# Performance work log

Measured on AMD Instinct MI355X. Metric: run time of the kernel, lower is better.

The kernel has to match this reference:

```python
import jax, jax.numpy as jnp
import numpy as np

N_GRAPHS = 128
NEG_SLOPE = 0.2
BN_EPS = 1e-5


def _gatv2(x, edge_index, edge_attr, Wl, bl, Wr, br, We, att, bias):
    # PyG GATv2Conv, heads=1, add_self_loops=True with fill_value='mean' for edge_attr.
    N = x.shape[0]
    src, dst = edge_index[0], edge_index[1]
    ones = jnp.ones(src.shape[0], dtype=x.dtype)
    deg = jax.ops.segment_sum(ones, dst, num_segments=N)
    loop_attr = jax.ops.segment_sum(edge_attr, dst, num_segments=N) / jnp.maximum(deg, 1.0)[:, None]
    idx = jnp.arange(N)
    src = jnp.concatenate([src, idx])
    dst = jnp.concatenate([dst, idx])
    ea = jnp.concatenate([edge_attr, loop_attr], axis=0)
    xl = x @ Wl + bl            # source projection [N, out]
    xr = x @ Wr + br            # target projection [N, out]
    h = jax.nn.leaky_relu(xl[src] + xr[dst] + ea @ We, NEG_SLOPE)  # [E, out]
    e = h @ att                 # attention logits [E]
    m = jax.ops.segment_max(e, dst, num_segments=N)
    ex = jnp.exp(e - m[dst])
    den = jax.ops.segment_sum(ex, dst, num_segments=N)
    alpha = ex / den[dst]       # per-destination softmax
    out = jax.ops.segment_sum(xl[src] * alpha[:, None], dst, num_segments=N)
    return out + bias


def setup_inputs() -> dict:
    key = jax.random.key(0)
    ks = jax.random.split(key, 32)
    N, E, FIN, ED = 16384, 131072, 256, 32

    def lin(k, fi, fo):
        return jax.random.normal(k, (fi, fo), jnp.float32) / np.sqrt(fi)

    d = {}
    d['x'] = jax.random.normal(ks[0], (N, FIN), jnp.float32)
    d['edge_index'] = jax.random.randint(ks[1], (2, E), 0, N)
    d['edge_attr'] = jax.random.normal(ks[2], (E, ED), jnp.float32)
    d['batch'] = jnp.sort(jax.random.randint(ks[3], (N,), 0, N_GRAPHS))
    dims = [(FIN, 512), (512, 1024), (1024, 256)]
    ki = 4
    for i, (fi, fo) in enumerate(dims, 1):
        d[f'Wl{i}'] = lin(ks[ki], fi, fo); ki += 1
        d[f'bl{i}'] = jnp.zeros((fo,), jnp.float32)
        d[f'Wr{i}'] = lin(ks[ki], fi, fo); ki += 1
        d[f'br{i}'] = jnp.zeros((fo,), jnp.float32)
        d[f'We{i}'] = lin(ks[ki], ED, fo); ki += 1
        d[f'att{i}'] = jax.random.normal(ks[ki], (fo,), jnp.float32) / np.sqrt(fo); ki += 1
        d[f'bc{i}'] = jnp.zeros((fo,), jnp.float32)
    d['fc1_w'] = lin(ks[ki], 256, 64); ki += 1
    d['fc1_b'] = jnp.zeros((64,), jnp.float32)
    d['bn_g'] = jnp.ones((64,), jnp.float32)
    d['bn_b'] = jnp.zeros((64,), jnp.float32)
    d['fc2_w'] = lin(ks[ki], 64, 1); ki += 1
    d['fc2_b'] = jnp.zeros((1,), jnp.float32)
    return d


def reference(x, edge_index, edge_attr, batch,
              Wl1, bl1, Wr1, br1, We1, att1, bc1,
              Wl2, bl2, Wr2, br2, We2, att2, bc2,
              Wl3, bl3, Wr3, br3, We3, att3, bc3,
              fc1_w, fc1_b, bn_g, bn_b, fc2_w, fc2_b):
    h = jax.nn.relu(_gatv2(x, edge_index, edge_attr, Wl1, bl1, Wr1, br1, We1, att1, bc1))
    h = jax.nn.relu(_gatv2(h, edge_index, edge_attr, Wl2, bl2, Wr2, br2, We2, att2, bc2))
    h = jax.nn.relu(_gatv2(h, edge_index, edge_attr, Wl3, bl3, Wr3, br3, We3, att3, bc3))
    # global mean pool over graphs
    cnt = jax.ops.segment_sum(jnp.ones(h.shape[0], h.dtype), batch, num_segments=N_GRAPHS)
    pooled = jax.ops.segment_sum(h, batch, num_segments=N_GRAPHS) / jnp.maximum(cnt, 1.0)[:, None]
    # dropout in eval mode (identity)
    z = pooled @ fc1_w + fc1_b
    mu = jnp.mean(z, axis=0)
    var = jnp.var(z, axis=0)
    z = (z - mu) / jnp.sqrt(var + BN_EPS) * bn_g + bn_b
    z = jax.nn.relu(z)
    return z @ fc2_w + fc2_b
```

## Files before the change

kernel.cpp:

```cpp
#include <hip/hip_runtime.h>
#include <hip/hip_bf16.h>
#include <math.h>

#define NEG_SLOPE 0.2f

typedef short bf16x8 __attribute__((ext_vector_type(8)));
typedef float f32x4 __attribute__((ext_vector_type(4)));

__device__ __forceinline__ float lrelu(float x){ return x >= 0.f ? x : NEG_SLOPE * x; }
__device__ __forceinline__ unsigned short f2bf(float f){
  __hip_bfloat16 h = __float2bfloat16(f);
  return *(unsigned short*)&h;
}
__device__ __forceinline__ float bf2f(unsigned short u){
  return __uint_as_float((unsigned)u << 16);
}
__device__ __forceinline__ void up8(uint4 q, float* f){
  f[0] = __uint_as_float(q.x << 16); f[1] = __uint_as_float(q.x & 0xffff0000u);
  f[2] = __uint_as_float(q.y << 16); f[3] = __uint_as_float(q.y & 0xffff0000u);
  f[4] = __uint_as_float(q.z << 16); f[5] = __uint_as_float(q.z & 0xffff0000u);
  f[6] = __uint_as_float(q.w << 16); f[7] = __uint_as_float(q.w & 0xffff0000u);
}

__device__ __forceinline__ void gload_lds16(const unsigned short* g, unsigned short* l){
  __builtin_amdgcn_global_load_lds(
      (const __attribute__((address_space(1))) unsigned int*)g,
      (__attribute__((address_space(3))) unsigned int*)l, 16, 0, 0);
}

__global__ void k_deg(const int* __restrict__ ei, int* __restrict__ deg, int E){
  int e = blockIdx.x * 256 + threadIdx.x;
  if (e >= E) return;
  atomicAdd(&deg[ei[E + e]], 1);
}

__global__ void k_scan(const int* __restrict__ deg, int* __restrict__ row_start, int N){
  __shared__ int s[256];
  int t = threadIdx.x;
  int base = t * 64;
  int sum = 0;
  for (int i = 0; i < 64; ++i) sum += deg[base + i] + 1;
  s[t] = sum;
  __syncthreads();
  for (int off = 1; off < 256; off <<= 1){
    int v = (t >= off) ? s[t - off] : 0;
    __syncthreads();
    s[t] += v;
    __syncthreads();
  }
  int run = s[t] - sum;
  for (int i = 0; i < 64; ++i){ row_start[base + i] = run; run += deg[base + i] + 1; }
  if (t == 255) row_start[N] = run;
}

__global__ void k_csr_build(const int* __restrict__ ei, const int* __restrict__ row_start,
                            int* __restrict__ fill, int* __restrict__ csr_src,
                            int* __restrict__ csr_eid, int* __restrict__ csr_dst,
                            int N, int E){
  int idx = blockIdx.x * 256 + threadIdx.x;
  if (idx < N){
    int p = row_start[idx];
    csr_src[p] = idx;
    csr_eid[p] = E;
    csr_dst[p] = idx;
  } else {
    int e = idx - N;
    if (e >= E) return;
    int dst = ei[E + e];
    int p = row_start[dst] + 1 + atomicAdd(&fill[dst], 1);
    csr_src[p] = ei[e];
    csr_eid[p] = e;
    csr_dst[p] = dst;
  }
}

__global__ void k_eaprep(const float* __restrict__ ea, const int* __restrict__ csr_eid,
                         const int* __restrict__ row_start,
                         unsigned short* __restrict__ ea_perm, int N, int Eaug, int E){
  int idx = blockIdx.x * 256 + threadIdx.x;
  if (idx < N * 32){
    int n = idx >> 5, k = idx & 31;
    int rs = row_start[n], re = row_start[n + 1];
    float sum = 0.f;
    for (int i = rs + 1; i < re; ++i)
      sum += ea[(size_t)csr_eid[i] * 32 + k];
    float d = (float)max(re - rs - 1, 1);
    ea_perm[(size_t)rs * 32 + k] = f2bf(sum / d);
  } else {
    int j = idx - N * 32;
    int p = j >> 3, q = j & 7;
    if (p >= Eaug) return;
    int e = csr_eid[p];
    if (e >= E) return;
    float4 v = ((const float4*)(ea + (size_t)e * 32))[q];
    ushort4 o;
    o.x = f2bf(v.x); o.y = f2bf(v.y); o.z = f2bf(v.z); o.w = f2bf(v.w);
    *(ushort4*)&ea_perm[(size_t)p * 32 + q * 4] = o;
  }
}

__global__ void k_cvt_bf16(const float* __restrict__ in, unsigned short* __restrict__ out, int n4){
  int idx = blockIdx.x * 256 + threadIdx.x;
  if (idx >= n4) return;
  float4 v = *(const float4*)&in[idx * 4];
  ushort4 o;
  o.x = f2bf(v.x); o.y = f2bf(v.y); o.z = f2bf(v.z); o.w = f2bf(v.w);
  *(ushort4*)&out[idx * 4] = o;
}

__global__ __launch_bounds__(256) void k_transpose2_bf16(const float* __restrict__ W0,
    const float* __restrict__ W1, unsigned short* __restrict__ Wt0,
    unsigned short* __restrict__ Wt1, int K, int N){
  __shared__ float tile[64][65];
  const float* W = blockIdx.z ? W1 : W0;
  unsigned short* Wt = blockIdx.z ? Wt1 : Wt0;
  int n0 = blockIdx.x * 64, k0 = blockIdx.y * 64;
  int col = threadIdx.x & 63, rq = threadIdx.x >> 6;
  #pragma unroll
  for (int i = 0; i < 16; ++i){
    int r = rq * 16 + i;
    tile[r][col] = W[(size_t)(k0 + r) * N + n0 + col];
  }
  __syncthreads();
  #pragma unroll
  for (int i = 0; i < 16; ++i){
    int r = rq * 16 + i;
    Wt[(size_t)(n0 + r) * K + k0 + col] = f2bf(tile[col][r]);
  }
}

__global__ void k_transpose_we(const float* __restrict__ We, unsigned short* __restrict__ WeT, int FO){
  int idx = blockIdx.x * 256 + threadIdx.x;
  if (idx >= 32 * FO) return;
  int k = idx / FO, n = idx % FO;
  WeT[n * 32 + k] = f2bf(We[idx]);
}

__global__ void k_mfma_gemm2(const unsigned short* __restrict__ A,
    const unsigned short* __restrict__ BtL, const unsigned short* __restrict__ BtR,
    const float* __restrict__ biasL, const float* __restrict__ biasR,
    unsigned short* __restrict__ CL, unsigned short* __restrict__ CR, int FO, int K){
  __shared__ unsigned short lds[16384];
  unsigned short* As0 = lds;
  unsigned short* As1 = lds + 4096;
  unsigned short* Bs0 = lds + 8192;
  unsigned short* Bs1 = lds + 12288;
  const unsigned short* Bt = blockIdx.z ? BtR : BtL;
  const float* bias = blockIdx.z ? biasR : biasL;
  unsigned short* C = blockIdx.z ? CR : CL;
  int t = threadIdx.x;
  int mb = blockIdx.x, nb = blockIdx.y;
  int lane = t & 63, w = t >> 6;
  int wm = (w & 1) * 64, wn = (w >> 1) * 64;
  int lo = lane & 15, hi = lane >> 4;
  int srow = w * 32 + (lane >> 2);
  int scol = (lane & 3) * 8;
  const unsigned short* Ap0 = A + (size_t)(mb * 128 + srow) * K + scol;
  const unsigned short* Ap1 = Ap0 + (size_t)16 * K;
  const unsigned short* Bp0 = Bt + (size_t)(nb * 128 + srow) * K + scol;
  const unsigned short* Bp1 = Bp0 + (size_t)16 * K;
  unsigned short* Ad00 = As0 + (w * 32) * 32;
  unsigned short* Ad01 = As0 + (w * 32 + 16) * 32;
  unsigned short* Ad10 = As1 + (w * 32) * 32;
  unsigned short* Ad11 = As1 + (w * 32 + 16) * 32;
  unsigned short* Bd00 = Bs0 + (w * 32) * 32;
  unsigned short* Bd01 = Bs0 + (w * 32 + 16) * 32;
  unsigned short* Bd10 = Bs1 + (w * 32) * 32;
  unsigned short* Bd11 = Bs1 + (w * 32 + 16) * 32;
  f32x4 acc[4][4] = {};
  for (int k0 = 0; k0 < K; k0 += 64){
    gload_lds16(Ap0 + k0, Ad00);
    gload_lds16(Ap1 + k0, Ad01);
    gload_lds16(Ap0 + k0 + 32, Ad10);
    gload_lds16(Ap1 + k0 + 32, Ad11);
    gload_lds16(Bp0 + k0, Bd00);
    gload_lds16(Bp1 + k0, Bd01);
    gload_lds16(Bp0 + k0 + 32, Bd10);
    gload_lds16(Bp1 + k0 + 32, Bd11);
    __syncthreads();
    #pragma unroll
    for (int ks = 0; ks < 2; ++ks){
      const unsigned short* Asx = ks ? As1 : As0;
      const unsigned short* Bsx = ks ? Bs1 : Bs0;
      bf16x8 af[4], bfr[4];
      #pragma unroll
      for (int i = 0; i < 4; ++i){
        af[i]  = *(const bf16x8*)&Asx[(wm + i * 16 + lo) * 32 + hi * 8];
        bfr[i] = *(const bf16x8*)&Bsx[(wn + i * 16 + lo) * 32 + hi * 8];
      }
      #pragma unroll
      for (int mi = 0; mi < 4; ++mi)
        #pragma unroll
        for (int ni = 0; ni < 4; ++ni)
          acc[mi][ni] = __builtin_amdgcn_mfma_f32_16x16x32_bf16(af[mi], bfr[ni], acc[mi][ni], 0, 0, 0);
    }
    __syncthreads();
  }
  #pragma unroll
  for (int ni = 0; ni < 4; ++ni){
    int col = wn + ni * 16 + lo;
    float bv = bias[nb * 128 + col];
    #pragma unroll
    for (int mi = 0; mi < 4; ++mi){
      int row = wm + mi * 16 + hi * 4;
      #pragma unroll
      for (int r = 0; r < 4; ++r)
        lds[(row + r) * 128 + col] = f2bf(acc[mi][ni][r] + bv);
    }
  }
  __syncthreads();
  #pragma unroll
  for (int q = 0; q < 8; ++q){
    int idx = q * 256 + t;
    int row = idx >> 4;
    int cs = (idx & 15) * 8;
    *(float4*)&C[(size_t)(mb * 128 + row) * FO + nb * 128 + cs] = *(float4*)&lds[row * 128 + cs];
  }
}

template<int TILES>
__global__ __launch_bounds__(256, 3) void k_logit(const unsigned short* __restrict__ Ap,
    const unsigned short* __restrict__ WeT, const unsigned short* __restrict__ XL,
    const unsigned short* __restrict__ XRb, const int* __restrict__ csr_src,
    const int* __restrict__ csr_dst, const float* __restrict__ att,
    float* __restrict__ logit){
  const int FO = TILES * 128;
  const int EWS = 140;
  __shared__ unsigned short ewt[128 * EWS];
  __shared__ int s_soff[128], s_doff[128];
  int t = threadIdx.x;
  int base = blockIdx.x * 128;
  if (t < 128){
    s_soff[t] = csr_src[base + t] * FO;
    s_doff[t] = csr_dst[base + t] * FO;
  }
  int lane = t & 63, w = t >> 6;
  int wm = (w & 1) * 64, wn = (w >> 1) * 64;
  int lo = lane & 15, hi = lane >> 4;
  bf16x8 af[4];
  #pragma unroll
  for (int i = 0; i < 4; ++i)
    af[i] = *(const bf16x8*)&Ap[(size_t)(base + wm + i * 16 + lo) * 32 + hi * 8];
  int grp = t >> 4, li = t & 15;
  __syncthreads();
  int soff8[8], doff8[8];
  #pragma unroll
  for (int e8 = 0; e8 < 8; ++e8){
    soff8[e8] = s_soff[grp * 8 + e8] + li * 8;
    doff8[e8] = s_doff[grp * 8 + e8] + li * 8;
  }
  float part[8] = {};
  #pragma unroll 1
  for (int nb = 0; nb < TILES; ++nb){
    bf16x8 bfr[4];
    #pragma unroll
    for (int i = 0; i < 4; ++i)
      bfr[i] = *(const bf16x8*)&WeT[(size_t)(nb * 128 + wn + i * 16 + lo) * 32 + hi * 8];
    __syncthreads();
    #pragma unroll
    for (int ni = 0; ni < 4; ++ni){
      f32x4 acc[4] = {};
      #pragma unroll
      for (int mi = 0; mi < 4; ++mi)
        acc[mi] = __builtin_amdgcn_mfma_f32_16x16x32_bf16(af[mi], bfr[ni], acc[mi], 0, 0, 0);
      int col = wn + ni * 16 + lo;
      #pragma unroll
      for (int mi = 0; mi < 4; ++mi){
        int row = wm + mi * 16 + hi * 4;
        #pragma unroll
        for (int r = 0; r < 4; ++r)
          ewt[(row + r) * EWS + col] = f2bf(acc[mi][r]);
      }
    }
    __syncthreads();
    float4 aA = *(const float4*)&att[nb * 128 + li * 8];
    float4 aB = *(const float4*)&att[nb * 128 + li * 8 + 4];
    #pragma unroll
    for (int e8 = 0; e8 < 8; ++e8){
      int r = grp * 8 + e8;
      uint4 qx = *(const uint4*)&XL [(size_t)soff8[e8] + nb * 128];
      uint4 qr = *(const uint4*)&XRb[(size_t)doff8[e8] + nb * 128];
      uint4 qe = *(const uint4*)&ewt[r * EWS + li * 8];
      float fx[8], fr8[8], fe[8];
      up8(qx, fx); up8(qr, fr8); up8(qe, fe);
      float s;
      s  = aA.x * lrelu(fx[0] + fr8[0] + fe[0]);
      s += aA.y * lrelu(fx[1] + fr8[1] + fe[1]);
      s += aA.z * lrelu(fx[2] + fr8[2] + fe[2]);
      s += aA.w * lrelu(fx[3] + fr8[3] + fe[3]);
      s += aB.x * lrelu(fx[4] + fr8[4] + fe[4]);
      s += aB.y * lrelu(fx[5] + fr8[5] + fe[5]);
      s += aB.z * lrelu(fx[6] + fr8[6] + fe[6]);
      s += aB.w * lrelu(fx[7] + fr8[7] + fe[7]);
      part[e8] += s;
    }
  }
  #pragma unroll
  for (int e8 = 0; e8 < 8; ++e8){
    float v = part[e8];
    v += __shfl_xor(v, 1, 64);
    v += __shfl_xor(v, 2, 64);
    v += __shfl_xor(v, 4, 64);
    v += __shfl_xor(v, 8, 64);
    if (li == 0) logit[base + grp * 8 + e8] = v;
  }
}

template<int CHUNKS, int VEC, typename OutT>
__global__ __launch_bounds__(256) void k_agg(const unsigned short* __restrict__ XL,
    const float* __restrict__ logit, const int* __restrict__ csr_src,
    const int* __restrict__ row_start, const float* __restrict__ bc,
    OutT* __restrict__ out){
  const int FO = CHUNKS * 64 * VEC;
  int lane = threadIdx.x & 63;
  int wave = threadIdx.x >> 6;
  int n = blockIdx.x * 4 + wave;
  int rs = row_start[n], re = row_start[n + 1];
  int jj = lane * VEC;
  float m = -1e30f;
  for (int i = rs; i < re; ++i) m = fmaxf(m, logit[i]);
  float acc[CHUNKS][VEC];
  #pragma unroll
  for (int c = 0; c < CHUNKS; ++c)
    #pragma unroll
    for (int v = 0; v < VEC; ++v) acc[c][v] = 0.f;
  float den = 0.f;
  int s_cur = csr_src[rs];
  float l_cur = logit[rs];
  for (int i = rs; i < re; ++i){
    float f = __expf(l_cur - m);
    int s = s_cur;
    if (i + 1 < re){ s_cur = csr_src[i + 1]; l_cur = logit[i + 1]; }
    den += f;
    const unsigned short* xp = XL + (size_t)s * FO;
    #pragma unroll
    for (int c = 0; c < CHUNKS; ++c){
      int base = c * 64 * VEC + jj;
      float xl[VEC];
      if (VEC == 8){
        uint4 q = *(const uint4*)&xp[base];
        xl[0] = __uint_as_float(q.x << 16); xl[1] = __uint_as_float(q.x & 0xffff0000u);
        xl[2] = __uint_as_float(q.y << 16); xl[3] = __uint_as_float(q.y & 0xffff0000u);
        xl[4] = __uint_as_float(q.z << 16); xl[5] = __uint_as_float(q.z & 0xffff0000u);
        xl[6] = __uint_as_float(q.w << 16); xl[7] = __uint_as_float(q.w & 0xffff0000u);
      } else {
        ushort4 u = *(const ushort4*)&xp[base];
        xl[0] = bf2f(u.x); xl[1] = bf2f(u.y); xl[2] = bf2f(u.z); xl[3] = bf2f(u.w);
      }
      #pragma unroll
      for (int v = 0; v < VEC; ++v) acc[c][v] += f * xl[v];
    }
  }
  float inv = 1.f / den;
  #pragma unroll
  for (int c = 0; c < CHUNKS; ++c){
    int base = c * 64 * VEC + jj;
    #pragma unroll
    for (int v = 0; v < VEC; ++v){
      float b = bc[base + v];
      float o = fmaxf(acc[c][v] * inv + b, 0.f);
      if (sizeof(OutT) == 4) ((float*)out)[(size_t)n * FO + base + v] = o;
      else ((unsigned short*)out)[(size_t)n * FO + base + v] = f2bf(o);
    }
  }
}

__global__ void k_pool_part(const float* __restrict__ H, const int* __restrict__ batch,
                            float* __restrict__ partial, int N){
  __shared__ int se[2];
  int g = blockIdx.x, part = blockIdx.y;
  int t = threadIdx.x;
  if (t < 2){
    int target = g + t;
    int lo = 0, hi = N;
    while (lo < hi){ int mid = (lo + hi) >> 1; if (batch[mid] < target) lo = mid + 1; else hi = mid; }
    se[t] = lo;
  }
  __syncthreads();
  int s = se[0], e = se[1];
  int len = e - s;
  int p0 = s + (int)((long)len * part / 8);
  int p1 = s + (int)((long)len * (part + 1) / 8);
  float a = 0.f;
  for (int n = p0; n < p1; ++n) a += H[(size_t)n * 256 + t];
  partial[((size_t)g * 8 + part) * 256 + t] = a;
}

__global__ void k_fc1b(const float* __restrict__ partial, const int* __restrict__ batch,
                       const float* __restrict__ w, const float* __restrict__ b,
                       float* __restrict__ z, int N){
  __shared__ float ps[256];
  __shared__ int se[2];
  int g = blockIdx.x;
  int t = threadIdx.x;
  if (t < 2){
    int target = g + t;
    int lo = 0, hi = N;
    while (lo < hi){ int mid = (lo + hi) >> 1; if (batch[mid] < target) lo = mid + 1; else hi = mid; }
    se[t] = lo;
  }
  float a = 0.f;
  #pragma unroll
  for (int p = 0; p < 8; ++p) a += partial[((size_t)g * 8 + p) * 256 + t];
  ps[t] = a;
  __syncthreads();
  if (t < 64){
    float acc = 0.f;
    for (int k = 0; k < 256; ++k) acc += ps[k] * w[k * 64 + t];
    z[g * 64 + t] = acc / fmaxf((float)(se[1] - se[0]), 1.f) + b[t];
  }
}

__global__ void k_head(const float* __restrict__ z, const float* __restrict__ bn_g,
                       const float* __restrict__ bn_b, const float* __restrict__ w2,
                       const float* __restrict__ b2, float* __restrict__ out){
  __shared__ float mu_s[64], is_s[64];
  int t = threadIdx.x;
  if (t < 64){
    float mu = 0.f, m2 = 0.f;
    for (int g = 0; g < 128; ++g){ float v = z[g * 64 + t]; mu += v; m2 += v * v; }
    mu /= 128.f; m2 /= 128.f;
    float var = m2 - mu * mu;
    mu_s[t] = mu;
    is_s[t] = rsqrtf(var + 1e-5f);
  }
  __syncthreads();
  float o = b2[0];
  for (int j = 0; j < 64; ++j){
    float v = (z[t * 64 + j] - mu_s[j]) * is_s[j] * bn_g[j] + bn_b[j];
    o += fmaxf(v, 0.f) * w2[j];
  }
  out[t] = o;
}

extern "C" void kernel_launch(void* const* d_in, const int* in_sizes, int n_in,
                              void* d_out, int out_size, void* d_ws, size_t ws_size,
                              hipStream_t stream){
  const int N = 16384, E = 131072, Eaug = E + N, NG = 128;
  const float* x     = (const float*)d_in[0];
  const int*   ei    = (const int*)  d_in[1];
  const float* ea    = (const float*)d_in[2];
  const int*   batch = (const int*)  d_in[3];
  const float* Wl[3]  = {(const float*)d_in[4],  (const float*)d_in[11], (const float*)d_in[18]};
  const float* bl[3]  = {(const float*)d_in[5],  (const float*)d_in[12], (const float*)d_in[19]};
  const float* Wr[3]  = {(const float*)d_in[6],  (const float*)d_in[13], (const float*)d_in[20]};
  const float* br[3]  = {(const float*)d_in[7],  (const float*)d_in[14], (const float*)d_in[21]};
  const float* We[3]  = {(const float*)d_in[8],  (const float*)d_in[15], (const float*)d_in[22]};
  const float* att[3] = {(const float*)d_in[9],  (const float*)d_in[16], (const float*)d_in[23]};
  const float* bc[3]  = {(const float*)d_in[10], (const float*)d_in[17], (const float*)d_in[24]};
  const float* fc1_w = (const float*)d_in[25];
  const float* fc1_b = (const float*)d_in[26];
  const float* bn_g  = (const float*)d_in[27];
  const float* bn_b  = (const float*)d_in[28];
  const float* fc2_w = (const float*)d_in[29];
  const float* fc2_b = (const float*)d_in[30];
  float* out = (float*)d_out;

  char* wsb = (char*)d_ws;
  size_t off = 0;
  auto alloc = [&](size_t bytes) -> char* {
    char* p = wsb + off;
    off = (off + bytes + 255) & ~(size_t)255;
    return p;
  };
  int*   deg       = (int*)  alloc((size_t)N * 4);
  int*   fill      = (int*)  alloc((size_t)N * 4);
  int*   row_start = (int*)  alloc((size_t)(N + 1) * 4);
  int*   csr_src   = (int*)  alloc((size_t)Eaug * 4);
  int*   csr_eid   = (int*)  alloc((size_t)Eaug * 4);
  int*   csr_dst   = (int*)  alloc((size_t)Eaug * 4);
  float* logits    = (float*)alloc((size_t)Eaug * 4);
  unsigned short* ea_perm = (unsigned short*)alloc((size_t)Eaug * 32 * 2);
  unsigned short* XL   = (unsigned short*)alloc((size_t)N * 1024 * 2);
  unsigned short* XRb  = (unsigned short*)alloc((size_t)N * 1024 * 2);
  unsigned short* bufA = (unsigned short*)alloc((size_t)N * 1024 * 2);
  unsigned short* bufB = (unsigned short*)alloc((size_t)N * 512 * 4);
  unsigned short* WtL  = (unsigned short*)alloc((size_t)1024 * 1024 * 2);
  unsigned short* WtR  = (unsigned short*)alloc((size_t)1024 * 1024 * 2);
  unsigned short* WeT  = (unsigned short*)alloc((size_t)1024 * 32 * 2);
  float* ppart     = (float*)alloc((size_t)NG * 8 * 256 * 4);
  float* zbuf      = (float*)alloc((size_t)NG * 64 * 4);

  hipMemsetAsync(deg, 0, (size_t)2 * N * 4, stream);

  k_deg<<<E / 256, 256, 0, stream>>>(ei, deg, E);
  k_scan<<<1, 256, 0, stream>>>(deg, row_start, N);
  k_csr_build<<<(N + E) / 256, 256, 0, stream>>>(ei, row_start, fill, csr_src, csr_eid, csr_dst, N, E);
  k_eaprep<<<(N * 32 + Eaug * 8 + 255) / 256, 256, 0, stream>>>(ea, csr_eid, row_start, ea_perm, N, Eaug, E);
  k_cvt_bf16<<<(N * 256 / 4) / 256, 256, 0, stream>>>(x, bufA, N * 256 / 4);

  const int fin[3] = {256, 512, 1024};
  const int fo[3]  = {512, 1024, 256};
  const unsigned short* Ain[3] = {bufA, bufB, bufA};

  for (int L = 0; L < 3; ++L){
    int FI = fin[L], FO = fo[L];
    k_transpose2_bf16<<<dim3(FO / 64, FI / 64, 2), 256, 0, stream>>>(Wl[L], Wr[L], WtL, WtR, FI, FO);
    k_transpose_we<<<(32 * FO + 255) / 256, 256, 0, stream>>>(We[L], WeT, FO);
    dim3 gg(N / 128, FO / 128, 2);
    k_mfma_gemm2<<<gg, 256, 0, stream>>>(Ain[L], WtL, WtR, bl[L], br[L], XL, XRb, FO, FI);

    if (FO == 512){
      k_logit<4><<<Eaug / 128, 256, 0, stream>>>(ea_perm, WeT, XL, XRb, csr_src, csr_dst, att[L], logits);
      k_agg<1, 8, unsigned short><<<N / 4, 256, 0, stream>>>(XL, logits, csr_src, row_start, bc[L], bufB);
    } else if (FO == 1024){
      k_logit<8><<<Eaug / 128, 256, 0, stream>>>(ea_perm, WeT, XL, XRb, csr_src, csr_dst, att[L], logits);
      k_agg<2, 8, unsigned short><<<N / 4, 256, 0, stream>>>(XL, logits, csr_src, row_start, bc[L], bufA);
    } else {
      k_logit<2><<<Eaug / 128, 256, 0, stream>>>(ea_perm, WeT, XL, XRb, csr_src, csr_dst, att[L], logits);
      k_agg<1, 4, float><<<N / 4, 256, 0, stream>>>(XL, logits, csr_src, row_start, bc[L], (float*)bufB);
    }
  }

  k_pool_part<<<dim3(NG, 8), 256, 0, stream>>>((const float*)bufB, batch, ppart, N);
  k_fc1b<<<NG, 256, 0, stream>>>(ppart, batch, fc1_w, fc1_b, zbuf, N);
  k_head<<<1, 128, 0, stream>>>(zbuf, bn_g, bn_b, fc2_w, fc2_b, out);
}
```

Baseline: 581.0 us.

## Make k_logit per-wave independent, removing block-level barriers

Restructures the edge-logit kernel so each wave owns 32 edges and computes their edge-attribute projection for all 128 columns of a tile into a private LDS slice. Block-wide __syncthreads are replaced by a wave-local lgkmcnt wait. Source and destination offsets now move through lane shuffles instead of shared memory. This removes barrier stalls between the MFMA phase and the gather phase, at the cost of each wave loading the full WeT tile (8 fragments instead of 4), which raises register pressure.

```diff
diff --git a/kernel.cpp b/kernel.cpp
--- a/kernel.cpp
+++ b/kernel.cpp
@@ -226,61 +226,56 @@
     float* __restrict__ logit){
   const int FO = TILES * 128;
   const int EWS = 140;
-  __shared__ unsigned short ewt[128 * EWS];
-  __shared__ int s_soff[128], s_doff[128];
+  __shared__ unsigned short ewt[4 * 32 * EWS];
   int t = threadIdx.x;
   int base = blockIdx.x * 128;
-  if (t < 128){
-    s_soff[t] = csr_src[base + t] * FO;
-    s_doff[t] = csr_dst[base + t] * FO;
-  }
   int lane = t & 63, w = t >> 6;
-  int wm = (w & 1) * 64, wn = (w >> 1) * 64;
   int lo = lane & 15, hi = lane >> 4;
-  bf16x8 af[4];
-  #pragma unroll
-  for (int i = 0; i < 4; ++i)
-    af[i] = *(const bf16x8*)&Ap[(size_t)(base + wm + i * 16 + lo) * 32 + hi * 8];
-  int grp = t >> 4, li = t & 15;
-  __syncthreads();
+  unsigned short* ewt_w = ewt + w * 32 * EWS;
+  int ebase = base + w * 32;
+  int myS = csr_src[ebase + (lane & 31)] * FO;
+  int myD = csr_dst[ebase + (lane & 31)] * FO;
   int soff8[8], doff8[8];
   #pragma unroll
   for (int e8 = 0; e8 < 8; ++e8){
-    soff8[e8] = s_soff[grp * 8 + e8] + li * 8;
-    doff8[e8] = s_doff[grp * 8 + e8] + li * 8;
-  }
+    soff8[e8] = __shfl(myS, hi * 8 + e8, 64) + lo * 8;
+    doff8[e8] = __shfl(myD, hi * 8 + e8, 64) + lo * 8;
+  }
+  bf16x8 af[2];
+  #pragma unroll
+  for (int mi = 0; mi < 2; ++mi)
+    af[mi] = *(const bf16x8*)&Ap[(size_t)(ebase + mi * 16 + lo) * 32 + hi * 8];
   float part[8] = {};
   #pragma unroll 1
   for (int nb = 0; nb < TILES; ++nb){
-    bf16x8 bfr[4];
-    #pragma unroll
-    for (int i = 0; i < 4; ++i)
-      bfr[i] = *(const bf16x8*)&WeT[(size_t)(nb * 128 + wn + i * 16 + lo) * 32 + hi * 8];
-    __syncthreads();
-    #pragma unroll
-    for (int ni = 0; ni < 4; ++ni){
-      f32x4 acc[4] = {};
+    bf16x8 bfr[8];
+    #pragma unroll
+    for (int ci = 0; ci < 8; ++ci)
+      bfr[ci] = *(const bf16x8*)&WeT[(size_t)(nb * 128 + ci * 16 + lo) * 32 + hi * 8];
+    #pragma unroll
+    for (int ci = 0; ci < 8; ++ci){
+      f32x4 acc[2] = {};
       #pragma unroll
-      for (int mi = 0; mi < 4; ++mi)
-        acc[mi] = __builtin_amdgcn_mfma_f32_16x16x32_bf16(af[mi], bfr[ni], acc[mi], 0, 0, 0);
-      int col = wn + ni * 16 + lo;
+      for (int mi = 0; mi < 2; ++mi)
+        acc[mi] = __builtin_amdgcn_mfma_f32_16x16x32_bf16(af[mi], bfr[ci], acc[mi], 0, 0, 0);
+      int col = ci * 16 + lo;
       #pragma unroll
-      for (int mi = 0; mi < 4; ++mi){
-        int row = wm + mi * 16 + hi * 4;
+      for (int mi = 0; mi < 2; ++mi){
+        int row = mi * 16 + hi * 4;
         #pragma unroll
         for (int r = 0; r < 4; ++r)
-          ewt[(row + r) * EWS + col] = f2bf(acc[mi][r]);
+          ewt_w[(row + r) * EWS + col] = f2bf(acc[mi][r]);
       }
     }
-    __syncthreads();
-    float4 aA = *(const float4*)&att[nb * 128 + li * 8];
-    float4 aB = *(const float4*)&att[nb * 128 + li * 8 + 4];
+    asm volatile("s_waitcnt lgkmcnt(0)" ::: "memory");
+    float4 aA = *(const float4*)&att[nb * 128 + lo * 8];
+    float4 aB = *(const float4*)&att[nb * 128 + lo * 8 + 4];
     #pragma unroll
     for (int e8 = 0; e8 < 8; ++e8){
-      int r = grp * 8 + e8;
+      int r = hi * 8 + e8;
       uint4 qx = *(const uint4*)&XL [(size_t)soff8[e8] + nb * 128];
       uint4 qr = *(const uint4*)&XRb[(size_t)doff8[e8] + nb * 128];
-      uint4 qe = *(const uint4*)&ewt[r * EWS + li * 8];
+      uint4 qe = *(const uint4*)&ewt_w[r * EWS + lo * 8];
       float fx[8], fr8[8], fe[8];
       up8(qx, fx); up8(qr, fr8); up8(qe, fe);
       float s;
@@ -302,7 +297,7 @@
     v += __shfl_xor(v, 2, 64);
     v += __shfl_xor(v, 4, 64);
     v += __shfl_xor(v, 8, 64);
-    if (li == 0) logit[base + grp * 8 + e8] = v;
+    if (lo == 0) logit[ebase + hi * 8 + e8] = v;
   }
 }
 
```

Result: slower. 701.7 us (+20.8%).
